# Performance work log

Measured on AMD Instinct MI355X. Metric: run time of the kernel, lower is better.

The kernel has to match this reference:

```python
import jax, jax.numpy as jnp
import numpy as np

EPS = 6.4 / 255.0  # HistoGAN EPS
H_BINS = 64
SIGMA = 0.02


def rgb_uv_hist(x):
    """Differentiable RGB-uv histogram, x: [B,3,H,W] in [0,1]. Returns [B,3,h,h]."""
    x = jnp.clip(x, 0.0, 1.0)
    B = x.shape[0]
    I = x.reshape(B, 3, -1).transpose(0, 2, 1)  # [B, N, 3]
    Iy = jnp.sqrt(jnp.sum(I * I, axis=-1) + EPS)  # [B, N] intensity scale
    logI = jnp.log(I + EPS)  # [B, N, 3]
    delta = jnp.linspace(-3.0, 3.0, H_BINS, dtype=x.dtype)  # bin centers [h]

    def kernel(d):
        # inverse-quadratic: 1 / (1 + (|d - delta| / sigma)^2), d: [B,N] -> [B,N,h]
        diff = jnp.abs(d[..., None] - delta)
        return 1.0 / (1.0 + (diff * diff) / (SIGMA * SIGMA))

    # channel c uses u = log(c) - log(other1), v = log(c) - log(other2)
    chans = [(0, 1, 2), (1, 0, 2), (2, 0, 1)]
    hists = []
    for c, o1, o2 in chans:
        ku = kernel(logI[..., c] - logI[..., o1])  # [B,N,h]
        kv = kernel(logI[..., c] - logI[..., o2])  # [B,N,h]
        a = Iy[..., None] * ku  # [B,N,h]
        hists.append(jnp.einsum('bnu,bnv->buv', a, kv))  # [B,h,h]
    hists = jnp.stack(hists, axis=1)  # [B,3,h,h]
    norm = jnp.sum(hists, axis=(1, 2, 3), keepdims=True) + EPS
    return hists / norm


def setup_inputs() -> dict:
    key = jax.random.key(0)
    k1, k2 = jax.random.split(key)
    rgbd = jax.random.normal(k1, (8, 4, 256, 256), dtype=jnp.float32)
    th = jax.random.uniform(k2, (3, 64, 64), dtype=jnp.float32)
    th = th / jnp.sum(th)  # target histogram is a normalized distribution
    return {"rgbd": rgbd, "target_hist": th}


def reference(rgbd, target_hist):
    rgb = 0.5 * (rgbd[:, 0:3, :, :] + 1.0)
    hist = rgb_uv_hist(rgb)  # [B,3,64,64]
    # Hellinger-style histogram loss (HistoGAN histogram_loss)
    d = jnp.sqrt(target_hist) - jnp.sqrt(hist)
    loss = (1.0 / jnp.sqrt(2.0)) * jnp.sqrt(jnp.sum(d * d)) / hist.shape[0]
    return loss
```

## Files before the change

### kernel.cpp

```cpp
#include <hip/hip_runtime.h>
#include <hip/hip_bf16.h>
#include <math.h>

#define NPIX 65536
#define HEPS (6.4f / 255.0f)

typedef __bf16 bf16x8 __attribute__((ext_vector_type(8)));
typedef float  f32x4  __attribute__((ext_vector_type(4)));
typedef float  f32x2  __attribute__((ext_vector_type(2)));

__device__ __forceinline__ float clamp01(float x) { return fminf(fmaxf(x, 0.f), 1.f); }

template <int SEGB>
__global__ __launch_bounds__(256) void hist_mfma(const float* __restrict__ rgbd,
                                                 float* __restrict__ P,
                                                 float* __restrict__ ctrl) {
  constexpr int PPB = NPIX / SEGB;
  constexpr int NIT = PPB / 4 / 64;
  const int blk = blockIdx.x;
  const int seg = blk & (SEGB - 1);
  const int bc  = blk / SEGB;
  const int b = bc / 3;
  const int c = bc - 3 * b;
  const int t = threadIdx.x;
  const int l = t & 63;
  const int w = t >> 6;

  if (blk == 0 && t < 16) ctrl[t] = 0.f;

  __shared__ float stage[4][3][64];
  __shared__ f32x4 slab[2][16][64];

  const float* __restrict__ base = rgbd + (size_t)b * (4 * NPIX);

  f32x4 acc[16];
#pragma unroll
  for (int i = 0; i < 16; ++i) acc[i] = (f32x4){0.f, 0.f, 0.f, 0.f};

  const int halfq = l & 15;
  const int grp   = l >> 4;
  const float d50_0   = (-3.f + (float)halfq * (6.f / 63.f)) * 50.f;
  const float dstep50 = (16.f * 6.f / 63.f) * 50.f;
  const f32x2 one2 = {1.f, 1.f};

  const int p0 = seg * PPB + w * (PPB / 4);

  float pr = base[p0 + l];
  float pg = base[NPIX + p0 + l];
  float pb = base[2 * NPIX + p0 + l];

  for (int it = 0; it < NIT; ++it) {
    float r  = clamp01(fmaf(pr, 0.5f, 0.5f));
    float g  = clamp01(fmaf(pg, 0.5f, 0.5f));
    float bl = clamp01(fmaf(pb, 0.5f, 0.5f));
    float iy = sqrtf(fmaf(r, r, fmaf(g, g, fmaf(bl, bl, HEPS))));
    float lr = __logf(r + HEPS);
    float lg = __logf(g + HEPS);
    float lb = __logf(bl + HEPS);
    float u, v;
    if (c == 0)      { u = lr - lg; v = lr - lb; }
    else if (c == 1) { u = lg - lr; v = lg - lb; }
    else             { u = lb - lr; v = lb - lg; }
    stage[w][0][l] = u * 50.f;
    stage[w][1][l] = v * 50.f;
    stage[w][2][l] = iy;

    if (it + 1 < NIT) {
      const int p = p0 + (it + 1) * 64 + l;
      pr = base[p]; pg = base[NPIX + p]; pb = base[2 * NPIX + p];
    }
    asm volatile("s_waitcnt lgkmcnt(0)" ::: "memory");

#pragma unroll
    for (int s = 0; s < 2; ++s) {
      const int k0 = s * 32 + grp * 8;
      const f32x2* __restrict__ u2  = (const f32x2*)&stage[w][0][k0];
      const f32x2* __restrict__ v2  = (const f32x2*)&stage[w][1][k0];
      const f32x2* __restrict__ iy2 = (const f32x2*)&stage[w][2][k0];

      bf16x8 af[4];
#pragma unroll
      for (int ut = 0; ut < 4; ++ut) {
        const float dlt = d50_0 + (float)ut * dstep50;
        const f32x2 dlt2 = {dlt, dlt};
#pragma unroll
        for (int jp = 0; jp < 4; ++jp) {
          f32x2 x = u2[jp] - dlt2;
          f32x2 q = x * x + one2;
          f32x2 rc = {__builtin_amdgcn_rcpf(q[0]), __builtin_amdgcn_rcpf(q[1])};
          f32x2 a2 = iy2[jp] * rc;
          af[ut][2 * jp]     = (__bf16)a2[0];
          af[ut][2 * jp + 1] = (__bf16)a2[1];
        }
      }

#pragma unroll
      for (int vt = 0; vt < 4; ++vt) {
        const float dlt = d50_0 + (float)vt * dstep50;
        const f32x2 dlt2 = {dlt, dlt};
        bf16x8 bf;
#pragma unroll
        for (int jp = 0; jp < 4; ++jp) {
          f32x2 x = v2[jp] - dlt2;
          f32x2 q = x * x + one2;
          bf[2 * jp]     = (__bf16)__builtin_amdgcn_rcpf(q[0]);
          bf[2 * jp + 1] = (__bf16)__builtin_amdgcn_rcpf(q[1]);
        }
#pragma unroll
        for (int ut = 0; ut < 4; ++ut)
          acc[ut * 4 + vt] =
              __builtin_amdgcn_mfma_f32_16x16x32_bf16(af[ut], bf, acc[ut * 4 + vt], 0, 0, 0);
      }
    }
  }

  if (w >= 2) {
#pragma unroll
    for (int i = 0; i < 16; ++i) slab[w - 2][i][l] = acc[i];
  }
  __syncthreads();
  if (w < 2) {
#pragma unroll
    for (int i = 0; i < 16; ++i) acc[i] += slab[w][i][l];
  }
  __syncthreads();
  if (w == 1) {
#pragma unroll
    for (int i = 0; i < 16; ++i) slab[0][i][l] = acc[i];
  }
  __syncthreads();
  if (w == 0) {
    f32x4* __restrict__ Pv = (f32x4*)(P + (size_t)blk * 4096);
#pragma unroll
    for (int i = 0; i < 16; ++i) Pv[i * 64 + l] = acc[i] + slab[0][i][l];
  }
}

template <int SEGB>
__global__ __launch_bounds__(256) void reduce_partials(float* __restrict__ P,
                                                       float* __restrict__ norms) {
  const int e  = blockIdx.x * 256 + threadIdx.x;
  const int bc = e >> 12;
  const int si = e & 4095;
  float* __restrict__ p0 = P + (size_t)(bc * SEGB) * 4096 + si;
  float s = 0.f;
#pragma unroll
  for (int sg = 0; sg < SEGB; ++sg) s += p0[(size_t)sg * 4096];
  p0[0] = s;

  __shared__ float red[4];
  float ns = s;
#pragma unroll
  for (int off = 32; off > 0; off >>= 1) ns += __shfl_down(ns, off);
  if ((threadIdx.x & 63) == 0) red[threadIdx.x >> 6] = ns;
  __syncthreads();
  if (threadIdx.x == 0)
    atomicAdd(&norms[bc / 3], red[0] + red[1] + red[2] + red[3]);
}

template <int SEGB>
__global__ __launch_bounds__(256) void loss_final(const float* __restrict__ P,
                                                  const float* __restrict__ norms,
                                                  const float* __restrict__ th,
                                                  float* __restrict__ acc,
                                                  unsigned* __restrict__ counter,
                                                  float* __restrict__ out) {
  float s = 0.f;
  for (int idx = blockIdx.x * 256 + threadIdx.x; idx < 8 * 12288;
       idx += gridDim.x * 256) {
    const int b  = idx / 12288;
    const int r  = idx - b * 12288;
    const int c  = r >> 12;
    const int si = r & 4095;
    const int rg = si & 3;
    const int q  = si >> 2;
    const int l  = q & 63;
    const int i  = q >> 6;
    const int row = (i >> 2) * 16 + (l >> 4) * 4 + rg;
    const int col = (i & 3) * 16 + (l & 15);
    const float h = P[(size_t)((b * 3 + c) * SEGB) * 4096 + si] / (norms[b] + HEPS);
    const float d = sqrtf(th[c * 4096 + row * 64 + col]) - sqrtf(h);
    s += d * d;
  }
  __shared__ float red[4];
#pragma unroll
  for (int off = 32; off > 0; off >>= 1) s += __shfl_down(s, off);
  if ((threadIdx.x & 63) == 0) red[threadIdx.x >> 6] = s;
  __syncthreads();
  if (threadIdx.x == 0) {
    atomicAdd(acc, red[0] + red[1] + red[2] + red[3]);
    __threadfence();
    const unsigned old = atomicAdd(counter, 1u);
    if (old == (unsigned)(gridDim.x - 1)) {
      const float tot = atomicAdd(acc, 0.f);
      out[0] = sqrtf(tot) * 0.08838834764831845f;
    }
  }
}

template <int SEGB>
static void run_path(const float* rgbd, const float* th, float* out,
                     void* d_ws, hipStream_t stream) {
  const size_t nP = (size_t)24 * SEGB * 4096;
  float*    P       = (float*)d_ws;
  float*    ctrl    = P + nP;
  float*    norms   = ctrl;
  float*    acc     = ctrl + 8;
  unsigned* counter = (unsigned*)(ctrl + 9);

  hist_mfma<SEGB><<<24 * SEGB, 256, 0, stream>>>(rgbd, P, ctrl);
  reduce_partials<SEGB><<<384, 256, 0, stream>>>(P, norms);
  loss_final<SEGB><<<96, 256, 0, stream>>>(P, norms, th, acc, counter, out);
}

extern "C" void kernel_launch(void* const* d_in, const int* in_sizes, int n_in,
                              void* d_out, int out_size, void* d_ws, size_t ws_size,
                              hipStream_t stream) {
  const float* rgbd = (const float*)d_in[0];
  const float* th   = (const float*)d_in[1];
  float* out = (float*)d_out;

  const size_t need64 = ((size_t)24 * 64 * 4096 + 64) * sizeof(float);
  if (ws_size >= need64)
    run_path<64>(rgbd, th, out, d_ws, stream);
  else
    run_path<32>(rgbd, th, out, d_ws, stream);
}
```

Measured before the change: 126.1 us.

## Fuse three channel histograms per block and share kernel matrices via LDS

Each block now processes all three channels for a batch segment, with 384 threads. Kernel values for the three log-ratio differences are computed once into LDS bf16 matrices. Sign symmetry (bin reversal) lets each difference serve two channels, so the per-pixel rcp work shrinks relative to recomputing u/v per channel. Pixel loading and log computation are double-buffered in a dedicated wave, at the cost of extra barriers per 64-pixel chunk and LDS traffic for the MFMA operands.

```diff
diff --git a/kernel.cpp b/kernel.cpp
--- a/kernel.cpp
+++ b/kernel.cpp
@@ -4,148 +4,181 @@
 
 #define NPIX 65536
 #define HEPS (6.4f / 255.0f)
+#define LN2_50 34.65735902799726f
 
 typedef __bf16 bf16x8 __attribute__((ext_vector_type(8)));
 typedef float  f32x4  __attribute__((ext_vector_type(4)));
-typedef float  f32x2  __attribute__((ext_vector_type(2)));
+
+#define ROWS 72
+#define MATS (64 * ROWS)
 
 __device__ __forceinline__ float clamp01(float x) { return fminf(fmaxf(x, 0.f), 1.f); }
 
-template <int SEGB>
-__global__ __launch_bounds__(256) void hist_mfma(const float* __restrict__ rgbd,
-                                                 float* __restrict__ P,
-                                                 float* __restrict__ ctrl) {
-  constexpr int PPB = NPIX / SEGB;
-  constexpr int NIT = PPB / 4 / 64;
+template <int SEG>
+__global__ __launch_bounds__(384, 3) void hist_fused(const float* __restrict__ rgbd,
+                                                     float* __restrict__ P,
+                                                     float* __restrict__ ctrl) {
+  constexpr int PPB = NPIX / SEG;
+  constexpr int NCH = PPB / 64;
   const int blk = blockIdx.x;
-  const int seg = blk & (SEGB - 1);
-  const int bc  = blk / SEGB;
-  const int b = bc / 3;
-  const int c = bc - 3 * b;
+  const int seg = blk & (SEG - 1);
+  const int b   = blk / SEG;
   const int t = threadIdx.x;
   const int l = t & 63;
   const int w = t >> 6;
-
-  if (blk == 0 && t < 16) ctrl[t] = 0.f;
-
-  __shared__ float stage[4][3][64];
-  __shared__ f32x4 slab[2][16][64];
-
-  const float* __restrict__ base = rgbd + (size_t)b * (4 * NPIX);
-
-  f32x4 acc[16];
-#pragma unroll
-  for (int i = 0; i < 16; ++i) acc[i] = (f32x4){0.f, 0.f, 0.f, 0.f};
-
+  const int ch  = w >> 1;
+  const int pxh = w & 1;
   const int halfq = l & 15;
   const int grp   = l >> 4;
-  const float d50_0   = (-3.f + (float)halfq * (6.f / 63.f)) * 50.f;
-  const float dstep50 = (16.f * 6.f / 63.f) * 50.f;
-  const f32x2 one2 = {1.f, 1.f};
-
-  const int p0 = seg * PPB + w * (PPB / 4);
-
-  float pr = base[p0 + l];
-  float pg = base[NPIX + p0 + l];
-  float pb = base[2 * NPIX + p0 + l];
-
-  for (int it = 0; it < NIT; ++it) {
-    float r  = clamp01(fmaf(pr, 0.5f, 0.5f));
-    float g  = clamp01(fmaf(pg, 0.5f, 0.5f));
-    float bl = clamp01(fmaf(pb, 0.5f, 0.5f));
-    float iy = sqrtf(fmaf(r, r, fmaf(g, g, fmaf(bl, bl, HEPS))));
-    float lr = __logf(r + HEPS);
-    float lg = __logf(g + HEPS);
-    float lb = __logf(bl + HEPS);
-    float u, v;
-    if (c == 0)      { u = lr - lg; v = lr - lb; }
-    else if (c == 1) { u = lg - lr; v = lg - lb; }
-    else             { u = lb - lr; v = lb - lg; }
-    stage[w][0][l] = u * 50.f;
-    stage[w][1][l] = v * 50.f;
-    stage[w][2][l] = iy;
-
-    if (it + 1 < NIT) {
-      const int p = p0 + (it + 1) * 64 + l;
+
+  if (blk == 0 && t < 16) ctrl[t] = 0.f;
+
+  __shared__ __align__(16) __bf16 kmat[6 * MATS];
+  __shared__ __align__(16) float dst[2][4][64];
+
+  const float* __restrict__ base = rgbd + (size_t)b * (4 * NPIX);
+  const int pbase = seg * PPB;
+
+  const int mrow = t >> 7;
+  const int ebin = (t >> 1) & 63;
+  const int eph  = t & 1;
+  const float delta50 = (-3.f + (float)ebin * (6.f / 63.f)) * 50.f;
+
+  f32x4 acc[16];
+#pragma unroll
+  for (int i = 0; i < 16; ++i) acc[i] = (f32x4){0.f, 0.f, 0.f, 0.f};
+
+  if (t >= 320) {
+    const int p = pbase + l;
+    const float pr = base[p], pg = base[NPIX + p], pb = base[2 * NPIX + p];
+    const float r  = clamp01(fmaf(pr, 0.5f, 0.5f));
+    const float g  = clamp01(fmaf(pg, 0.5f, 0.5f));
+    const float bl = clamp01(fmaf(pb, 0.5f, 0.5f));
+    const float iy = sqrtf(fmaf(r, r, fmaf(g, g, fmaf(bl, bl, HEPS))));
+    const float a = __log2f(r + HEPS), bq = __log2f(g + HEPS), cq = __log2f(bl + HEPS);
+    dst[0][0][l] = (a - bq) * LN2_50;
+    dst[0][1][l] = (a - cq) * LN2_50;
+    dst[0][2][l] = (bq - cq) * LN2_50;
+    dst[0][3][l] = iy;
+  }
+  __syncthreads();
+
+  for (int ck = 0; ck < NCH; ++ck) {
+    const int cur = ck & 1;
+    float pr = 0.f, pg = 0.f, pb = 0.f;
+    const bool pre = (t >= 320) && (ck + 1 < NCH);
+    if (pre) {
+      const int p = pbase + (ck + 1) * 64 + l;
       pr = base[p]; pg = base[NPIX + p]; pb = base[2 * NPIX + p];
     }
-    asm volatile("s_waitcnt lgkmcnt(0)" ::: "memory");
-
-#pragma unroll
-    for (int s = 0; s < 2; ++s) {
-      const int k0 = s * 32 + grp * 8;
-      const f32x2* __restrict__ u2  = (const f32x2*)&stage[w][0][k0];
-      const f32x2* __restrict__ v2  = (const f32x2*)&stage[w][1][k0];
-      const f32x2* __restrict__ iy2 = (const f32x2*)&stage[w][2][k0];
-
-      bf16x8 af[4];
-#pragma unroll
-      for (int ut = 0; ut < 4; ++ut) {
-        const float dlt = d50_0 + (float)ut * dstep50;
-        const f32x2 dlt2 = {dlt, dlt};
-#pragma unroll
-        for (int jp = 0; jp < 4; ++jp) {
-          f32x2 x = u2[jp] - dlt2;
-          f32x2 q = x * x + one2;
-          f32x2 rc = {__builtin_amdgcn_rcpf(q[0]), __builtin_amdgcn_rcpf(q[1])};
-          f32x2 a2 = iy2[jp] * rc;
-          af[ut][2 * jp]     = (__bf16)a2[0];
-          af[ut][2 * jp + 1] = (__bf16)a2[1];
+
+    {
+      const f32x4* __restrict__ dr = (const f32x4*)&dst[cur][mrow][eph * 32];
+      const f32x4* __restrict__ ir = (const f32x4*)&dst[cur][3][eph * 32];
+      const int pxo = eph * 32;
+      __bf16* __restrict__ m0 = kmat + (size_t)(mrow * 2)     * MATS;
+      __bf16* __restrict__ m1 = kmat + (size_t)(mrow * 2 + 1) * MATS;
+      const int rA = ebin * ROWS + pxo;
+      const int rR = (63 - ebin) * ROWS + pxo;
+#pragma unroll
+      for (int g = 0; g < 4; ++g) {
+        const f32x4 dA = dr[2 * g], dB = dr[2 * g + 1];
+        const f32x4 xA = dA - delta50, xB = dB - delta50;
+        float k[8];
+#pragma unroll
+        for (int e = 0; e < 4; ++e) {
+          k[e]     = __builtin_amdgcn_rcpf(fmaf(xA[e], xA[e], 1.f));
+          k[e + 4] = __builtin_amdgcn_rcpf(fmaf(xB[e], xB[e], 1.f));
+        }
+        if (mrow == 2) {
+          bf16x8 pk;
+#pragma unroll
+          for (int e = 0; e < 8; ++e) pk[e] = (__bf16)k[e];
+          *(bf16x8*)&m0[rA + g * 8] = pk;
+          *(bf16x8*)&m1[rR + g * 8] = pk;
+        } else {
+          const f32x4 iA = ir[2 * g], iB = ir[2 * g + 1];
+          bf16x8 wg;
+#pragma unroll
+          for (int e = 0; e < 4; ++e) {
+            wg[e]     = (__bf16)(iA[e] * k[e]);
+            wg[e + 4] = (__bf16)(iB[e] * k[e + 4]);
+          }
+          if (mrow == 0) {
+            *(bf16x8*)&m0[rA + g * 8] = wg;
+            *(bf16x8*)&m1[rR + g * 8] = wg;
+          } else {
+            bf16x8 pk;
+#pragma unroll
+            for (int e = 0; e < 8; ++e) pk[e] = (__bf16)k[e];
+            *(bf16x8*)&m0[rA + g * 8] = pk;
+            *(bf16x8*)&m1[rR + g * 8] = wg;
+          }
         }
       }
-
-#pragma unroll
-      for (int vt = 0; vt < 4; ++vt) {
-        const float dlt = d50_0 + (float)vt * dstep50;
-        const f32x2 dlt2 = {dlt, dlt};
-        bf16x8 bf;
-#pragma unroll
-        for (int jp = 0; jp < 4; ++jp) {
-          f32x2 x = v2[jp] - dlt2;
-          f32x2 q = x * x + one2;
-          bf[2 * jp]     = (__bf16)__builtin_amdgcn_rcpf(q[0]);
-          bf[2 * jp + 1] = (__bf16)__builtin_amdgcn_rcpf(q[1]);
-        }
-#pragma unroll
-        for (int ut = 0; ut < 4; ++ut)
+    }
+
+    if (pre) {
+      const float r  = clamp01(fmaf(pr, 0.5f, 0.5f));
+      const float g  = clamp01(fmaf(pg, 0.5f, 0.5f));
+      const float bl = clamp01(fmaf(pb, 0.5f, 0.5f));
+      const float iy = sqrtf(fmaf(r, r, fmaf(g, g, fmaf(bl, bl, HEPS))));
+      const float a = __log2f(r + HEPS), bq = __log2f(g + HEPS), cq = __log2f(bl + HEPS);
+      dst[cur ^ 1][0][l] = (a - bq) * LN2_50;
+      dst[cur ^ 1][1][l] = (a - cq) * LN2_50;
+      dst[cur ^ 1][2][l] = (bq - cq) * LN2_50;
+      dst[cur ^ 1][3][l] = iy;
+    }
+    __syncthreads();
+
+    {
+      const __bf16* __restrict__ Am;
+      const __bf16* __restrict__ Bm;
+      if (ch == 0)      { Am = kmat + 0 * MATS; Bm = kmat + 2 * MATS; }
+      else if (ch == 1) { Am = kmat + 1 * MATS; Bm = kmat + 4 * MATS; }
+      else              { Am = kmat + 3 * MATS; Bm = kmat + 5 * MATS; }
+      const int kpx = pxh * 32 + grp * 8;
+      bf16x8 bfv[4];
+#pragma unroll
+      for (int vt = 0; vt < 4; ++vt)
+        bfv[vt] = *(const bf16x8*)&Bm[(vt * 16 + halfq) * ROWS + kpx];
+#pragma unroll
+      for (int ut = 0; ut < 4; ++ut) {
+        const bf16x8 af = *(const bf16x8*)&Am[(ut * 16 + halfq) * ROWS + kpx];
+#pragma unroll
+        for (int vt = 0; vt < 4; ++vt)
           acc[ut * 4 + vt] =
-              __builtin_amdgcn_mfma_f32_16x16x32_bf16(af[ut], bf, acc[ut * 4 + vt], 0, 0, 0);
+              __builtin_amdgcn_mfma_f32_16x16x32_bf16(af, bfv[vt], acc[ut * 4 + vt], 0, 0, 0);
       }
     }
-  }
-
-  if (w >= 2) {
-#pragma unroll
-    for (int i = 0; i < 16; ++i) slab[w - 2][i][l] = acc[i];
-  }
-  __syncthreads();
-  if (w < 2) {
-#pragma unroll
-    for (int i = 0; i < 16; ++i) acc[i] += slab[w][i][l];
-  }
-  __syncthreads();
-  if (w == 1) {
-#pragma unroll
-    for (int i = 0; i < 16; ++i) slab[0][i][l] = acc[i];
-  }
-  __syncthreads();
-  if (w == 0) {
-    f32x4* __restrict__ Pv = (f32x4*)(P + (size_t)blk * 4096);
-#pragma unroll
-    for (int i = 0; i < 16; ++i) Pv[i * 64 + l] = acc[i] + slab[0][i][l];
-  }
-}
-
-template <int SEGB>
+    __syncthreads();
+  }
+
+  f32x4* __restrict__ slab = (f32x4*)kmat;
+  if (pxh == 1) {
+#pragma unroll
+    for (int i = 0; i < 16; ++i) slab[(ch * 16 + i) * 64 + l] = acc[i];
+  }
+  __syncthreads();
+  if (pxh == 0) {
+    f32x4* __restrict__ Pv = (f32x4*)(P + ((size_t)blk * 3 + ch) * 4096);
+#pragma unroll
+    for (int i = 0; i < 16; ++i) Pv[i * 64 + l] = acc[i] + slab[(ch * 16 + i) * 64 + l];
+  }
+}
+
+template <int SEG>
 __global__ __launch_bounds__(256) void reduce_partials(float* __restrict__ P,
                                                        float* __restrict__ norms) {
   const int e  = blockIdx.x * 256 + threadIdx.x;
   const int bc = e >> 12;
   const int si = e & 4095;
-  float* __restrict__ p0 = P + (size_t)(bc * SEGB) * 4096 + si;
+  const int b  = bc / 3;
+  const int c  = bc - 3 * b;
+  float* __restrict__ p0 = P + ((size_t)b * SEG * 3 + c) * 4096 + si;
   float s = 0.f;
 #pragma unroll
-  for (int sg = 0; sg < SEGB; ++sg) s += p0[(size_t)sg * 4096];
+  for (int sg = 0; sg < SEG; ++sg) s += p0[(size_t)sg * 3 * 4096];
   p0[0] = s;
 
   __shared__ float red[4];
@@ -155,10 +188,10 @@
   if ((threadIdx.x & 63) == 0) red[threadIdx.x >> 6] = ns;
   __syncthreads();
   if (threadIdx.x == 0)
-    atomicAdd(&norms[bc / 3], red[0] + red[1] + red[2] + red[3]);
-}
-
-template <int SEGB>
+    atomicAdd(&norms[b], red[0] + red[1] + red[2] + red[3]);
+}
+
+template <int SEG>
 __global__ __launch_bounds__(256) void loss_final(const float* __restrict__ P,
                                                   const float* __restrict__ norms,
                                                   const float* __restrict__ th,
@@ -178,7 +211,7 @@
     const int i  = q >> 6;
     const int row = (i >> 2) * 16 + (l >> 4) * 4 + rg;
     const int col = (i & 3) * 16 + (l & 15);
-    const float h = P[(size_t)((b * 3 + c) * SEGB) * 4096 + si] / (norms[b] + HEPS);
+    const float h = P[((size_t)b * SEG * 3 + c) * 4096 + si] / (norms[b] + HEPS);
     const float d = sqrtf(th[c * 4096 + row * 64 + col]) - sqrtf(h);
     s += d * d;
   }
@@ -198,19 +231,19 @@
   }
 }
 
-template <int SEGB>
+template <int SEG>
 static void run_path(const float* rgbd, const float* th, float* out,
                      void* d_ws, hipStream_t stream) {
-  const size_t nP = (size_t)24 * SEGB * 4096;
+  const size_t nP = (size_t)8 * SEG * 3 * 4096;
   float*    P       = (float*)d_ws;
   float*    ctrl    = P + nP;
   float*    norms   = ctrl;
   float*    acc     = ctrl + 8;
   unsigned* counter = (unsigned*)(ctrl + 9);
 
-  hist_mfma<SEGB><<<24 * SEGB, 256, 0, stream>>>(rgbd, P, ctrl);
-  reduce_partials<SEGB><<<384, 256, 0, stream>>>(P, norms);
-  loss_final<SEGB><<<96, 256, 0, stream>>>(P, norms, th, acc, counter, out);
+  hist_fused<SEG><<<8 * SEG, 384, 0, stream>>>(rgbd, P, ctrl);
+  reduce_partials<SEG><<<384, 256, 0, stream>>>(P, norms);
+  loss_final<SEG><<<96, 256, 0, stream>>>(P, norms, th, acc, counter, out);
 }
 
 extern "C" void kernel_launch(void* const* d_in, const int* in_sizes, int n_in,
@@ -220,7 +253,7 @@
   const float* th   = (const float*)d_in[1];
   float* out = (float*)d_out;
 
-  const size_t need64 = ((size_t)24 * 64 * 4096 + 64) * sizeof(float);
+  const size_t need64 = ((size_t)8 * 64 * 3 * 4096 + 64) * sizeof(float);
   if (ws_size >= need64)
     run_path<64>(rgbd, th, out, d_ws, stream);
   else
```

Result: slower. 141.8 us (+12.4%).
